# Optimization experiments

Hardware: AMD Instinct MI355X
Metric: run time of the kernel (lower is better)

The kernel has to match this reference:

```python
import jax, jax.numpy as jnp
import numpy as np

CONF_THRESHOLD = 0.25
IOU_THRESHOLD = 0.45
NUM_CLASSES = 18
TOPK = 300  # fixed candidate budget per class (jit-compatible replacement for boolean masking)


def setup_inputs() -> dict:
    key = jax.random.key(0)
    # raw head output [B, 4+num_classes, N_anchors]; wrapper permutes to [B, N, C]
    out = jax.random.normal(key, (32, 4 + NUM_CLASSES, 8400), dtype=jnp.float32)
    return {"out": out}


def _pairwise_iou(boxes):
    # boxes: [K, 4] in xyxy
    x1, y1, x2, y2 = boxes[:, 0], boxes[:, 1], boxes[:, 2], boxes[:, 3]
    area = jnp.clip(x2 - x1, 0.0) * jnp.clip(y2 - y1, 0.0)  # [K]
    ix1 = jnp.maximum(x1[:, None], x1[None, :])
    iy1 = jnp.maximum(y1[:, None], y1[None, :])
    ix2 = jnp.minimum(x2[:, None], x2[None, :])
    iy2 = jnp.minimum(y2[:, None], y2[None, :])
    inter = jnp.clip(ix2 - ix1, 0.0) * jnp.clip(iy2 - iy1, 0.0)  # [K, K]
    union = area[:, None] + area[None, :] - inter
    return inter / jnp.maximum(union, 1e-9)


def _nms_one_class(boxes_xyxy, class_scores):
    # boxes_xyxy: [N, 4], class_scores: [N]
    # conf-threshold masking -> fixed-size top-k candidate set (scores sorted desc)
    masked = jnp.where(class_scores > CONF_THRESHOLD, class_scores, -1.0)
    vals, idx = jax.lax.top_k(masked, TOPK)          # [K], [K]
    cboxes = boxes_xyxy[idx]                          # [K, 4]
    cvalid = vals > CONF_THRESHOLD                    # [K]
    iou = _pairwise_iou(cboxes)                       # [K, K]
    rng = jnp.arange(TOPK)

    # greedy NMS over score-sorted candidates: box i (if kept) suppresses later
    # boxes with IoU > threshold -- identical to torchvision.ops.nms semantics
    def body(i, keep):
        sup = (iou[i] > IOU_THRESHOLD) & keep[i] & (rng > i)
        return keep & ~sup

    keep = jax.lax.fori_loop(0, TOPK, body, cvalid)
    return cboxes, vals, keep


def reference(out):
    x = out.transpose(0, 2, 1)                        # [B, N, 4+nc]
    raw_boxes = x[..., :4]
    scores = jax.nn.sigmoid(x[..., 4:])               # [B, N, nc]
    cx, cy, w, h = raw_boxes[..., 0], raw_boxes[..., 1], raw_boxes[..., 2], raw_boxes[..., 3]
    boxes_xyxy = jnp.stack([cx - w / 2, cy - h / 2, cx + w / 2, cy + h / 2], axis=-1)  # [B, N, 4]

    def per_image(bx, sc):
        # vmap the per-class NMS loop (classes on axis 1 of sc)
        cboxes, vals, keep = jax.vmap(_nms_one_class, in_axes=(None, 1))(bx, sc)  # [nc, K, ...]
        cls_ids = jnp.broadcast_to(
            jnp.arange(NUM_CLASSES, dtype=bx.dtype)[:, None], (NUM_CLASSES, TOPK)
        )
        det = jnp.concatenate([cboxes, vals[..., None], cls_ids[..., None]], axis=-1)  # [nc, K, 6]
        det = det * keep[..., None].astype(det.dtype)  # zero out suppressed / below-conf rows
        return det.reshape(NUM_CLASSES * TOPK, 6)

    # [B, nc*K, 6]; fixed-shape padded equivalent of the variable-length detection lists
    return jax.vmap(per_image)(boxes_xyxy, scores)
```

## Files before the change

kernel.cpp:

```cpp
#include <hip/hip_runtime.h>
#include <cstdint>

#pragma clang fp contract(off)

#define NB      32
#define NC      18
#define NA      8400
#define NCH     (4 + NC)
#define NTASK   (NB * NC)
#define TOPK    300
#define TARGET  316
#define NBINS   2048
#define CAP     1024
#define CONF    0.25f
#define IOU_T   0.45f
#define NT      512
#define NW      (NT / 64)
#define PREF_X  1.4f
#define XHI     (-1.0984f)
#define XLO     (-1.0988f)

#define FAST_KBASE 0xBFB00000u
#define FAST_SHIFT 14
#define FB_KBASE   0x40000000u
#define FB_SHIFT   21

#define M45 (30198989.0 / 67108864.0)

typedef unsigned long long ull;

__device__ __forceinline__ float sigmoidf(float x) {
    return 1.0f / (1.0f + expf(-x));
}
__device__ __forceinline__ unsigned int mono_key(unsigned int bits) {
    return (bits & 0x80000000u) ? ~bits : (bits | 0x80000000u);
}
__device__ __forceinline__ unsigned int mono_inv(unsigned int key) {
    return (key & 0x80000000u) ? (key ^ 0x80000000u) : ~key;
}
__device__ __forceinline__ bool conf_pass(float x) {
    if (x >= XHI) return true;
    if (x <= XLO) return false;
    return sigmoidf(x) > CONF;
}
__device__ __forceinline__ unsigned int make_key(float x) {
    return conf_pass(x) ? mono_key(__float_as_uint(x)) : 0u;
}
__device__ __forceinline__ ull readlane64(ull v, int i) {
    unsigned lo = (unsigned)__builtin_amdgcn_readlane((int)(unsigned)(v & 0xFFFFFFFFull), i);
    unsigned hi = (unsigned)__builtin_amdgcn_readlane((int)(unsigned)(v >> 32), i);
    return ((ull)hi << 32) | (ull)lo;
}

__device__ __forceinline__ void suffix_find(unsigned int* hist, unsigned int* wtot,
                                            int target, int tid, int* s_T1) {
    const int base = tid * (NBINS / NT);
    unsigned int v = 0;
#pragma unroll
    for (int k = 0; k < NBINS / NT; ++k) v += hist[base + k];
    const int lane = tid & 63;
    unsigned int s = v;
#pragma unroll
    for (int d = 1; d < 64; d <<= 1) {
        unsigned int o = __shfl_down(s, d, 64);
        if (lane + d < 64) s += o;
    }
    if (lane == 0) wtot[tid >> 6] = s;
    __syncthreads();
    unsigned int above_waves = 0;
    for (int wv = (tid >> 6) + 1; wv < NW; ++wv) above_waves += wtot[wv];
    unsigned int acc = (s - v) + above_waves;
    for (int bin = base + (NBINS / NT) - 1; bin >= base; --bin) {
        unsigned int cnt = hist[bin];
        if (acc < (unsigned int)target && acc + cnt >= (unsigned int)target) *s_T1 = bin;
        acc += cnt;
    }
    __syncthreads();
}

#define OFF_CAND   8192
#define POOL1_BYTES 16384

#define PIN64(x) asm volatile("" : "+v"(x))

__global__ __launch_bounds__(NT, 4) void k_fused(const float* __restrict__ in,
                                                 float* __restrict__ out) {
    __shared__ __align__(16) unsigned char pool[POOL1_BYTES];
    __shared__ __align__(16) float4 sBox[TOPK];
    __shared__ float sVal[TOPK];
    __shared__ float sAr[TOPK];
    __shared__ unsigned int wtot[NW];
    __shared__ unsigned int s_cnt, s_cnt2;
    __shared__ int s_T1;

    unsigned int* hist = (unsigned int*)pool;
    ull* cand2 = (ull*)pool;
    ull* cand  = (ull*)(pool + OFF_CAND);
    ull* sSup  = (ull*)pool;

    const int tid = threadIdx.x;
    const int lane = tid & 63;
    const int wave = tid >> 6;
    const ull ltm = (1ull << lane) - 1ull;
    const int t = blockIdx.x;
    const int b = (t & 7) + 8 * ((t >> 3) & 3);
    const int c = t >> 5;
    const float* cls = in + (size_t)b * NCH * NA + (size_t)(4 + c) * NA;
    const float* box = in + (size_t)b * NCH * NA;

    for (int i = tid; i < NBINS; i += NT) hist[i] = 0;
    for (int r = tid; r < TOPK; r += NT) {
        sBox[r] = float4{0.f, 0.f, 0.f, 0.f};
        sVal[r] = 0.f;
        sAr[r] = 0.f;
    }
    if (tid == 0) { s_cnt = 0; s_cnt2 = 0; s_T1 = -1; }
    __syncthreads();

    {
        const float4* cls4 = (const float4*)cls;
        int q = tid;
        float4 v = cls4[q];
        while (true) {
            const int qn = q + NT;
            const bool more = qn < NA / 4;
            float4 vn;
            if (more) vn = cls4[qn];

            const unsigned int i0 = (unsigned int)q * 4u;
            float xs[4] = {v.x, v.y, v.z, v.w};
            ull m[4];
            unsigned int cnt = 0;
#pragma unroll
            for (int u = 0; u < 4; ++u) {
                m[u] = __ballot(xs[u] > PREF_X);
                cnt += (unsigned int)__popcll(m[u]);
            }
            if (cnt) {
                unsigned int base = 0;
                if (lane == 0) base = atomicAdd(&s_cnt, cnt);
                base = (unsigned int)__builtin_amdgcn_readfirstlane((int)base);
                unsigned int pre = 0;
#pragma unroll
                for (int u = 0; u < 4; ++u) {
                    if (xs[u] > PREF_X) {
                        unsigned int mk = mono_key(__float_as_uint(xs[u]));
                        atomicAdd(&hist[min((mk - FAST_KBASE) >> FAST_SHIFT,
                                            (unsigned)(NBINS - 1))], 1u);
                        unsigned int p = base + pre + (unsigned int)__popcll(m[u] & ltm);
                        if (p < CAP)
                            cand[p] = ((ull)mk << 32) | (ull)(~(i0 + u));
                    }
                    pre += (unsigned int)__popcll(m[u]);
                }
            }
            if (!more) break;
            v = vn; q = qn;
        }
    }
    __syncthreads();

    const int pcnt = (int)s_cnt;
    if (pcnt >= TARGET && pcnt <= CAP) {
        suffix_find(hist, wtot, TARGET, tid, &s_T1);
        const ull thr = ((ull)FAST_KBASE + ((ull)(unsigned int)s_T1 << FAST_SHIFT)) << 32;
        const int iters = (pcnt + NT - 1) / NT;
        for (int it = 0; it < iters; ++it) {
            int e = tid + it * NT;
            bool act = e < pcnt;
            ull k = act ? cand[e] : 0ull;
            bool sel = act && (k >= thr);
            ull mb = __ballot(sel);
            unsigned int cnt = (unsigned int)__popcll(mb);
            if (cnt) {
                unsigned int basep = 0;
                if (lane == 0) basep = atomicAdd(&s_cnt2, cnt);
                basep = (unsigned int)__builtin_amdgcn_readfirstlane((int)basep);
                if (sel) {
                    float xv = __uint_as_float(mono_inv((unsigned int)(k >> 32)));
                    float sv = sigmoidf(xv);
                    unsigned int p = basep + (unsigned int)__popcll(mb & ltm);
                    if (p < CAP)
                        cand2[p] = ((ull)__float_as_uint(sv) << 32) | (k & 0xFFFFFFFFull);
                }
            }
        }
        __syncthreads();
    } else {
        __syncthreads();
        for (int i = tid; i < NBINS; i += NT) hist[i] = 0;
        __syncthreads();
        {
            const float4* cls4 = (const float4*)cls;
            for (int q = tid; q < NA / 4; q += NT) {
                float4 v = cls4[q];
                unsigned int kx = make_key(v.x), ky = make_key(v.y);
                unsigned int kz = make_key(v.z), kw = make_key(v.w);
                if (kx) atomicAdd(&hist[min((kx - FB_KBASE) >> FB_SHIFT, (unsigned)(NBINS - 1))], 1u);
                if (ky) atomicAdd(&hist[min((ky - FB_KBASE) >> FB_SHIFT, (unsigned)(NBINS - 1))], 1u);
                if (kz) atomicAdd(&hist[min((kz - FB_KBASE) >> FB_SHIFT, (unsigned)(NBINS - 1))], 1u);
                if (kw) atomicAdd(&hist[min((kw - FB_KBASE) >> FB_SHIFT, (unsigned)(NBINS - 1))], 1u);
            }
        }
        __syncthreads();
        suffix_find(hist, wtot, TARGET, tid, &s_T1);
        {
            const ull thr = (s_T1 < 0) ? 0ull
                : ((ull)FB_KBASE + ((ull)(unsigned int)s_T1 << FB_SHIFT));
            const float4* cls4 = (const float4*)cls;
            for (int q = tid; q < NA / 4; q += NT) {
                float4 v = cls4[q];
                const unsigned int i0 = (unsigned int)q * 4u;
                float xs[4] = {v.x, v.y, v.z, v.w};
#pragma unroll
                for (int u = 0; u < 4; ++u) {
                    unsigned int d = make_key(xs[u]);
                    if (d && (ull)d >= thr) {
                        unsigned int p = atomicAdd(&s_cnt2, 1u);
                        if (p < CAP) {
                            float sv = sigmoidf(xs[u]);
                            cand2[p] = ((ull)__float_as_uint(sv) << 32) | (ull)(~(i0 + u));
                        }
                    }
                }
            }
        }
        __syncthreads();
    }

    const int F = min((int)s_cnt2, CAP);
    const int numSel = min(F, TOPK);

    for (int e = tid; e < F; e += NT) {
        ull k = cand2[e];
        int rank = 0;
        int o = 0;
#pragma unroll 2
        for (; o + 4 <= F; o += 4) {
            ulonglong2 p0 = *(const ulonglong2*)&cand2[o];
            ulonglong2 p1 = *(const ulonglong2*)&cand2[o + 2];
            rank += (p0.x > k) + (p0.y > k) + (p1.x > k) + (p1.y > k);
        }
        for (; o < F; ++o) rank += (cand2[o] > k) ? 1 : 0;
        if (rank < TOPK) {
            unsigned int i = ~(unsigned int)(k & 0xFFFFFFFFull);
            float cx = box[i];
            float cy = box[NA + i];
            float w  = box[2 * NA + i];
            float h  = box[3 * NA + i];
            float hw = w * 0.5f, hh = h * 0.5f;
            float x1 = cx - hw, y1 = cy - hh, x2 = cx + hw, y2 = cy + hh;
            sBox[rank] = float4{x1, y1, x2, y2};
            sVal[rank] = __uint_as_float((unsigned int)(k >> 32));
            sAr[rank] = fmaxf(x2 - x1, 0.f) * fmaxf(y2 - y1, 0.f);
        }
    }
    __syncthreads();

    float4 cb[5];
    float ca[5];
#pragma unroll
    for (int w = 0; w < 5; ++w) {
        int j = (w << 6) + lane;
        bool v = j < TOPK;
        cb[w] = v ? sBox[j] : float4{0.f, 0.f, 0.f, 0.f};
        ca[w] = v ? sAr[j] : 0.f;
    }
    for (int r = wave; r < TOPK; r += NW) {
        const bool vrow = r < numSel;
        float4 bi = sBox[r];
        float ai = sAr[r];
        const bool act = vrow && (ai > 0.0f);
        const int w0 = r >> 6;
#pragma unroll
        for (int w = 0; w < 5; ++w) {
            ull bal = 0ull;
            if (w >= w0 && act) {
                const int j = (w << 6) + lane;
                bool supb = false;
                if (j < numSel && j > r) {
                    float xx1 = fmaxf(bi.x, cb[w].x);
                    float yy1 = fmaxf(bi.y, cb[w].y);
                    float xx2 = fminf(bi.z, cb[w].z);
                    float yy2 = fminf(bi.w, cb[w].w);
                    float iw = fmaxf(xx2 - xx1, 0.0f);
                    float ih = fmaxf(yy2 - yy1, 0.0f);
                    float inter = iw * ih;
                    float un = ai + ca[w] - inter;
                    float D = fmaxf(un, 1e-9f);
                    supb = (double)inter > M45 * (double)D;
                }
                bal = __ballot(supb);
            }
            if (lane == 0) sSup[r * 5 + w] = bal;
        }
    }
    __syncthreads();

    if (wave != 0) return;

    ull rem0 = 0, rem1 = 0, rem2 = 0, rem3 = 0, rem4 = 0;
    {
        const ull* p = sSup + (size_t)lane * 5;
        ull B0 = p[0], B1 = p[1], B2 = p[2], B3 = p[3], B4 = p[4];
        PIN64(B0); PIN64(B1); PIN64(B2); PIN64(B3); PIN64(B4);
        ull nz = __ballot((B0 | B1 | B2 | B3 | B4) != 0ull);
        while (nz) {
            int i = __builtin_ctzll(nz);
            nz &= nz - 1;
            if (!((rem0 >> i) & 1ull)) {
                rem0 |= readlane64(B0, i); rem1 |= readlane64(B1, i);
                rem2 |= readlane64(B2, i); rem3 |= readlane64(B3, i);
                rem4 |= readlane64(B4, i);
            }
        }
    }
    {
        const ull* p = sSup + (size_t)(64 + lane) * 5;
        ull B0 = p[0], B1 = p[1], B2 = p[2], B3 = p[3], B4 = p[4];
        PIN64(B0); PIN64(B1); PIN64(B2); PIN64(B3); PIN64(B4);
        ull nz = __ballot((B0 | B1 | B2 | B3 | B4) != 0ull);
        while (nz) {
            int i = __builtin_ctzll(nz);
            nz &= nz - 1;
            if (!((rem1 >> i) & 1ull)) {
                rem0 |= readlane64(B0, i); rem1 |= readlane64(B1, i);
                rem2 |= readlane64(B2, i); rem3 |= readlane64(B3, i);
                rem4 |= readlane64(B4, i);
            }
        }
    }
    {
        const ull* p = sSup + (size_t)(128 + lane) * 5;
        ull B0 = p[0], B1 = p[1], B2 = p[2], B3 = p[3], B4 = p[4];
        PIN64(B0); PIN64(B1); PIN64(B2); PIN64(B3); PIN64(B4);
        ull nz = __ballot((B0 | B1 | B2 | B3 | B4) != 0ull);
        while (nz) {
            int i = __builtin_ctzll(nz);
            nz &= nz - 1;
            if (!((rem2 >> i) & 1ull)) {
                rem0 |= readlane64(B0, i); rem1 |= readlane64(B1, i);
                rem2 |= readlane64(B2, i); rem3 |= readlane64(B3, i);
                rem4 |= readlane64(B4, i);
            }
        }
    }
    {
        const ull* p = sSup + (size_t)(192 + lane) * 5;
        ull B0 = p[0], B1 = p[1], B2 = p[2], B3 = p[3], B4 = p[4];
        PIN64(B0); PIN64(B1); PIN64(B2); PIN64(B3); PIN64(B4);
        ull nz = __ballot((B0 | B1 | B2 | B3 | B4) != 0ull);
        while (nz) {
            int i = __builtin_ctzll(nz);
            nz &= nz - 1;
            if (!((rem3 >> i) & 1ull)) {
                rem0 |= readlane64(B0, i); rem1 |= readlane64(B1, i);
                rem2 |= readlane64(B2, i); rem3 |= readlane64(B3, i);
                rem4 |= readlane64(B4, i);
            }
        }
    }
    {
        const bool v4 = lane < (TOPK - 256);
        const ull* p = sSup + (size_t)(256 + (v4 ? lane : 0)) * 5;
        ull B0 = v4 ? p[0] : 0ull, B1 = v4 ? p[1] : 0ull, B2 = v4 ? p[2] : 0ull,
            B3 = v4 ? p[3] : 0ull, B4 = v4 ? p[4] : 0ull;
        PIN64(B0); PIN64(B1); PIN64(B2); PIN64(B3); PIN64(B4);
        ull nz = __ballot((B0 | B1 | B2 | B3 | B4) != 0ull);
        while (nz) {
            int i = __builtin_ctzll(nz);
            nz &= nz - 1;
            if (!((rem4 >> i) & 1ull)) {
                rem0 |= readlane64(B0, i); rem1 |= readlane64(B1, i);
                rem2 |= readlane64(B2, i); rem3 |= readlane64(B3, i);
                rem4 |= readlane64(B4, i);
            }
        }
    }

    float* outp = out + ((size_t)b * NC + c) * (TOPK * 6);
    auto write_row = [&](int w, ull remw) {
        int r = (w << 6) + lane;
        if (r < TOPK) {
            float x1 = 0.f, y1 = 0.f, x2 = 0.f, y2 = 0.f, vv = 0.f, cc = 0.f;
            if (r < numSel && ((~remw >> lane) & 1ull)) {
                float4 bb = sBox[r];
                x1 = bb.x; y1 = bb.y; x2 = bb.z; y2 = bb.w;
                vv = sVal[r]; cc = (float)c;
            }
            float* row = outp + r * 6;
            *(float2*)(row)     = float2{x1, y1};
            *(float2*)(row + 2) = float2{x2, y2};
            *(float2*)(row + 4) = float2{vv, cc};
        }
    };
    write_row(0, rem0);
    write_row(1, rem1);
    write_row(2, rem2);
    write_row(3, rem3);
    write_row(4, rem4);
}

extern "C" void kernel_launch(void* const* d_in, const int* in_sizes, int n_in,
                              void* d_out, int out_size, void* d_ws, size_t ws_size,
                              hipStream_t stream) {
    const float* in = (const float*)d_in[0];
    float* out = (float*)d_out;
    (void)d_ws; (void)ws_size;

    k_fused<<<NTASK, NT, 0, stream>>>(in, out);
}
```

Measured before the change: 102.1 us.

## Compact active NMS candidates before IoU matrix and parallelize output writes

Compacts the candidates with positive area into a dense list (actIdx/sPos) so the IoU bitmask and the greedy resolve cover only active boxes. Resolve chunks beyond nAct are skipped. Box loads are hoisted ahead of the rank loop so their latency overlaps it, and all threads now write output rows using the suppression mask shared through LDS. The cost is an extra compaction pass with two more barriers and a zero-init of sSup.

Result: faster. 86.28 us (-15.5%).

```diff
diff --git a/kernel.cpp b/kernel.cpp
--- a/kernel.cpp
+++ b/kernel.cpp
@@ -90,7 +90,10 @@
     __shared__ float sVal[TOPK];
     __shared__ float sAr[TOPK];
     __shared__ unsigned int wtot[NW];
-    __shared__ unsigned int s_cnt, s_cnt2;
+    __shared__ unsigned short actIdx[TOPK];
+    __shared__ unsigned short sPos[TOPK];
+    __shared__ ull s_remC[5];
+    __shared__ unsigned int s_cnt, s_cnt2, s_nAct;
     __shared__ int s_T1;
 
     unsigned int* hist = (unsigned int*)pool;
@@ -233,6 +236,11 @@
 
     for (int e = tid; e < F; e += NT) {
         ull k = cand2[e];
+        unsigned int i = ~(unsigned int)(k & 0xFFFFFFFFull);
+        float cx = box[i];
+        float cy = box[NA + i];
+        float w  = box[2 * NA + i];
+        float h  = box[3 * NA + i];
         int rank = 0;
         int o = 0;
 #pragma unroll 2
@@ -243,11 +251,6 @@
         }
         for (; o < F; ++o) rank += (cand2[o] > k) ? 1 : 0;
         if (rank < TOPK) {
-            unsigned int i = ~(unsigned int)(k & 0xFFFFFFFFull);
-            float cx = box[i];
-            float cy = box[NA + i];
-            float w  = box[2 * NA + i];
-            float h  = box[3 * NA + i];
             float hw = w * 0.5f, hh = h * 0.5f;
             float x1 = cx - hw, y1 = cy - hh, x2 = cx + hw, y2 = cy + hh;
             sBox[rank] = float4{x1, y1, x2, y2};
@@ -257,148 +260,180 @@
     }
     __syncthreads();
 
-    float4 cb[5];
-    float ca[5];
-#pragma unroll
-    for (int w = 0; w < 5; ++w) {
-        int j = (w << 6) + lane;
-        bool v = j < TOPK;
-        cb[w] = v ? sBox[j] : float4{0.f, 0.f, 0.f, 0.f};
-        ca[w] = v ? sAr[j] : 0.f;
-    }
-    for (int r = wave; r < TOPK; r += NW) {
-        const bool vrow = r < numSel;
-        float4 bi = sBox[r];
-        float ai = sAr[r];
-        const bool act = vrow && (ai > 0.0f);
-        const int w0 = r >> 6;
+    for (int i = tid; i < TOPK * 5; i += NT) sSup[i] = 0ull;
+    {
+        int r = tid;
+        bool act = (r < TOPK) && (r < numSel) && (sAr[r] > 0.0f);
+        ull mb = __ballot(act);
+        if (lane == 0) wtot[wave] = (unsigned int)__popcll(mb);
+        __syncthreads();
+        unsigned int basew = 0;
+        for (int w2 = 0; w2 < wave; ++w2) basew += wtot[w2];
+        if (tid == 0) {
+            unsigned int tot = 0;
+            for (int w2 = 0; w2 < NW; ++w2) tot += wtot[w2];
+            s_nAct = tot;
+        }
+        if (act) {
+            unsigned int p = basew + (unsigned int)__popcll(mb & ltm);
+            actIdx[p] = (unsigned short)r;
+            sPos[r] = (unsigned short)p;
+        }
+    }
+    __syncthreads();
+    const int nAct = (int)s_nAct;
+
+    {
+        float4 cb[5];
+        float ca[5];
 #pragma unroll
         for (int w = 0; w < 5; ++w) {
-            ull bal = 0ull;
-            if (w >= w0 && act) {
-                const int j = (w << 6) + lane;
-                bool supb = false;
-                if (j < numSel && j > r) {
-                    float xx1 = fmaxf(bi.x, cb[w].x);
-                    float yy1 = fmaxf(bi.y, cb[w].y);
-                    float xx2 = fminf(bi.z, cb[w].z);
-                    float yy2 = fminf(bi.w, cb[w].w);
-                    float iw = fmaxf(xx2 - xx1, 0.0f);
-                    float ih = fmaxf(yy2 - yy1, 0.0f);
-                    float inter = iw * ih;
-                    float un = ai + ca[w] - inter;
-                    float D = fmaxf(un, 1e-9f);
-                    supb = (double)inter > M45 * (double)D;
-                }
-                bal = __ballot(supb);
-            }
-            if (lane == 0) sSup[r * 5 + w] = bal;
-        }
-    }
-    __syncthreads();
-
-    if (wave != 0) return;
-
-    ull rem0 = 0, rem1 = 0, rem2 = 0, rem3 = 0, rem4 = 0;
+            int jc = (w << 6) + lane;
+            bool v = jc < nAct;
+            int j = v ? (int)actIdx[jc] : 0;
+            cb[w] = v ? sBox[j] : float4{0.f, 0.f, 0.f, 0.f};
+            ca[w] = v ? sAr[j] : 0.f;
+        }
+        const int wlast = (nAct > 0) ? ((nAct - 1) >> 6) : -1;
+        for (int p = wave; p < nAct; p += NW) {
+            int r = actIdx[p];
+            float4 bi = sBox[r];
+            float ai = sAr[r];
+            const int w0 = p >> 6;
+#pragma unroll
+            for (int w = 0; w < 5; ++w) {
+                if (w >= w0 && w <= wlast) {
+                    const int jc = (w << 6) + lane;
+                    bool supb = false;
+                    if (jc < nAct && jc > p) {
+                        float xx1 = fmaxf(bi.x, cb[w].x);
+                        float yy1 = fmaxf(bi.y, cb[w].y);
+                        float xx2 = fminf(bi.z, cb[w].z);
+                        float yy2 = fminf(bi.w, cb[w].w);
+                        float iw = fmaxf(xx2 - xx1, 0.0f);
+                        float ih = fmaxf(yy2 - yy1, 0.0f);
+                        float inter = iw * ih;
+                        float un = ai + ca[w] - inter;
+                        float D = fmaxf(un, 1e-9f);
+                        supb = (double)inter > M45 * (double)D;
+                    }
+                    ull bal = __ballot(supb);
+                    if (lane == 0) sSup[p * 5 + w] = bal;
+                }
+            }
+        }
+    }
+    __syncthreads();
+
+    if (wave == 0) {
+        ull rem0 = 0, rem1 = 0, rem2 = 0, rem3 = 0, rem4 = 0;
+        {
+            const ull* p = sSup + (size_t)lane * 5;
+            ull B0 = p[0], B1 = p[1], B2 = p[2], B3 = p[3], B4 = p[4];
+            PIN64(B0); PIN64(B1); PIN64(B2); PIN64(B3); PIN64(B4);
+            ull nz = __ballot((B0 | B1 | B2 | B3 | B4) != 0ull);
+            while (nz) {
+                int i = __builtin_ctzll(nz);
+                nz &= nz - 1;
+                if (!((rem0 >> i) & 1ull)) {
+                    rem0 |= readlane64(B0, i); rem1 |= readlane64(B1, i);
+                    rem2 |= readlane64(B2, i); rem3 |= readlane64(B3, i);
+                    rem4 |= readlane64(B4, i);
+                }
+            }
+        }
+        if (nAct > 64) {
+            const ull* p = sSup + (size_t)(64 + lane) * 5;
+            ull B0 = p[0], B1 = p[1], B2 = p[2], B3 = p[3], B4 = p[4];
+            PIN64(B0); PIN64(B1); PIN64(B2); PIN64(B3); PIN64(B4);
+            ull nz = __ballot((B0 | B1 | B2 | B3 | B4) != 0ull);
+            while (nz) {
+                int i = __builtin_ctzll(nz);
+                nz &= nz - 1;
+                if (!((rem1 >> i) & 1ull)) {
+                    rem0 |= readlane64(B0, i); rem1 |= readlane64(B1, i);
+                    rem2 |= readlane64(B2, i); rem3 |= readlane64(B3, i);
+                    rem4 |= readlane64(B4, i);
+                }
+            }
+        }
+        if (nAct > 128) {
+            const ull* p = sSup + (size_t)(128 + lane) * 5;
+            ull B0 = p[0], B1 = p[1], B2 = p[2], B3 = p[3], B4 = p[4];
+            PIN64(B0); PIN64(B1); PIN64(B2); PIN64(B3); PIN64(B4);
+            ull nz = __ballot((B0 | B1 | B2 | B3 | B4) != 0ull);
+            while (nz) {
+                int i = __builtin_ctzll(nz);
+                nz &= nz - 1;
+                if (!((rem2 >> i) & 1ull)) {
+                    rem0 |= readlane64(B0, i); rem1 |= readlane64(B1, i);
+                    rem2 |= readlane64(B2, i); rem3 |= readlane64(B3, i);
+                    rem4 |= readlane64(B4, i);
+                }
+            }
+        }
+        if (nAct > 192) {
+            const ull* p = sSup + (size_t)(192 + lane) * 5;
+            ull B0 = p[0], B1 = p[1], B2 = p[2], B3 = p[3], B4 = p[4];
+            PIN64(B0); PIN64(B1); PIN64(B2); PIN64(B3); PIN64(B4);
+            ull nz = __ballot((B0 | B1 | B2 | B3 | B4) != 0ull);
+            while (nz) {
+                int i = __builtin_ctzll(nz);
+                nz &= nz - 1;
+                if (!((rem3 >> i) & 1ull)) {
+                    rem0 |= readlane64(B0, i); rem1 |= readlane64(B1, i);
+                    rem2 |= readlane64(B2, i); rem3 |= readlane64(B3, i);
+                    rem4 |= readlane64(B4, i);
+                }
+            }
+        }
+        if (nAct > 256) {
+            const bool v4 = lane < (TOPK - 256);
+            const ull* p = sSup + (size_t)(256 + (v4 ? lane : 0)) * 5;
+            ull B0 = v4 ? p[0] : 0ull, B1 = v4 ? p[1] : 0ull, B2 = v4 ? p[2] : 0ull,
+                B3 = v4 ? p[3] : 0ull, B4 = v4 ? p[4] : 0ull;
+            PIN64(B0); PIN64(B1); PIN64(B2); PIN64(B3); PIN64(B4);
+            ull nz = __ballot((B0 | B1 | B2 | B3 | B4) != 0ull);
+            while (nz) {
+                int i = __builtin_ctzll(nz);
+                nz &= nz - 1;
+                if (!((rem4 >> i) & 1ull)) {
+                    rem0 |= readlane64(B0, i); rem1 |= readlane64(B1, i);
+                    rem2 |= readlane64(B2, i); rem3 |= readlane64(B3, i);
+                    rem4 |= readlane64(B4, i);
+                }
+            }
+        }
+        if (lane == 0) {
+            s_remC[0] = rem0; s_remC[1] = rem1; s_remC[2] = rem2;
+            s_remC[3] = rem3; s_remC[4] = rem4;
+        }
+    }
+    __syncthreads();
+
     {
-        const ull* p = sSup + (size_t)lane * 5;
-        ull B0 = p[0], B1 = p[1], B2 = p[2], B3 = p[3], B4 = p[4];
-        PIN64(B0); PIN64(B1); PIN64(B2); PIN64(B3); PIN64(B4);
-        ull nz = __ballot((B0 | B1 | B2 | B3 | B4) != 0ull);
-        while (nz) {
-            int i = __builtin_ctzll(nz);
-            nz &= nz - 1;
-            if (!((rem0 >> i) & 1ull)) {
-                rem0 |= readlane64(B0, i); rem1 |= readlane64(B1, i);
-                rem2 |= readlane64(B2, i); rem3 |= readlane64(B3, i);
-                rem4 |= readlane64(B4, i);
-            }
-        }
-    }
-    {
-        const ull* p = sSup + (size_t)(64 + lane) * 5;
-        ull B0 = p[0], B1 = p[1], B2 = p[2], B3 = p[3], B4 = p[4];
-        PIN64(B0); PIN64(B1); PIN64(B2); PIN64(B3); PIN64(B4);
-        ull nz = __ballot((B0 | B1 | B2 | B3 | B4) != 0ull);
-        while (nz) {
-            int i = __builtin_ctzll(nz);
-            nz &= nz - 1;
-            if (!((rem1 >> i) & 1ull)) {
-                rem0 |= readlane64(B0, i); rem1 |= readlane64(B1, i);
-                rem2 |= readlane64(B2, i); rem3 |= readlane64(B3, i);
-                rem4 |= readlane64(B4, i);
-            }
-        }
-    }
-    {
-        const ull* p = sSup + (size_t)(128 + lane) * 5;
-        ull B0 = p[0], B1 = p[1], B2 = p[2], B3 = p[3], B4 = p[4];
-        PIN64(B0); PIN64(B1); PIN64(B2); PIN64(B3); PIN64(B4);
-        ull nz = __ballot((B0 | B1 | B2 | B3 | B4) != 0ull);
-        while (nz) {
-            int i = __builtin_ctzll(nz);
-            nz &= nz - 1;
-            if (!((rem2 >> i) & 1ull)) {
-                rem0 |= readlane64(B0, i); rem1 |= readlane64(B1, i);
-                rem2 |= readlane64(B2, i); rem3 |= readlane64(B3, i);
-                rem4 |= readlane64(B4, i);
-            }
-        }
-    }
-    {
-        const ull* p = sSup + (size_t)(192 + lane) * 5;
-        ull B0 = p[0], B1 = p[1], B2 = p[2], B3 = p[3], B4 = p[4];
-        PIN64(B0); PIN64(B1); PIN64(B2); PIN64(B3); PIN64(B4);
-        ull nz = __ballot((B0 | B1 | B2 | B3 | B4) != 0ull);
-        while (nz) {
-            int i = __builtin_ctzll(nz);
-            nz &= nz - 1;
-            if (!((rem3 >> i) & 1ull)) {
-                rem0 |= readlane64(B0, i); rem1 |= readlane64(B1, i);
-                rem2 |= readlane64(B2, i); rem3 |= readlane64(B3, i);
-                rem4 |= readlane64(B4, i);
-            }
-        }
-    }
-    {
-        const bool v4 = lane < (TOPK - 256);
-        const ull* p = sSup + (size_t)(256 + (v4 ? lane : 0)) * 5;
-        ull B0 = v4 ? p[0] : 0ull, B1 = v4 ? p[1] : 0ull, B2 = v4 ? p[2] : 0ull,
-            B3 = v4 ? p[3] : 0ull, B4 = v4 ? p[4] : 0ull;
-        PIN64(B0); PIN64(B1); PIN64(B2); PIN64(B3); PIN64(B4);
-        ull nz = __ballot((B0 | B1 | B2 | B3 | B4) != 0ull);
-        while (nz) {
-            int i = __builtin_ctzll(nz);
-            nz &= nz - 1;
-            if (!((rem4 >> i) & 1ull)) {
-                rem0 |= readlane64(B0, i); rem1 |= readlane64(B1, i);
-                rem2 |= readlane64(B2, i); rem3 |= readlane64(B3, i);
-                rem4 |= readlane64(B4, i);
-            }
-        }
-    }
-
-    float* outp = out + ((size_t)b * NC + c) * (TOPK * 6);
-    auto write_row = [&](int w, ull remw) {
-        int r = (w << 6) + lane;
+        const int r = tid;
         if (r < TOPK) {
             float x1 = 0.f, y1 = 0.f, x2 = 0.f, y2 = 0.f, vv = 0.f, cc = 0.f;
-            if (r < numSel && ((~remw >> lane) & 1ull)) {
-                float4 bb = sBox[r];
-                x1 = bb.x; y1 = bb.y; x2 = bb.z; y2 = bb.w;
-                vv = sVal[r]; cc = (float)c;
-            }
+            if (r < numSel) {
+                bool sup = false;
+                if (sAr[r] > 0.0f) {
+                    int p = (int)sPos[r];
+                    sup = (s_remC[p >> 6] >> (p & 63)) & 1ull;
+                }
+                if (!sup) {
+                    float4 bb = sBox[r];
+                    x1 = bb.x; y1 = bb.y; x2 = bb.z; y2 = bb.w;
+                    vv = sVal[r]; cc = (float)c;
+                }
+            }
+            float* outp = out + ((size_t)b * NC + c) * (TOPK * 6);
             float* row = outp + r * 6;
             *(float2*)(row)     = float2{x1, y1};
             *(float2*)(row + 2) = float2{x2, y2};
             *(float2*)(row + 4) = float2{vv, cc};
         }
-    };
-    write_row(0, rem0);
-    write_row(1, rem1);
-    write_row(2, rem2);
-    write_row(3, rem3);
-    write_row(4, rem4);
+    }
 }
 
 extern "C" void kernel_launch(void* const* d_in, const int* in_sizes, int n_in,
```
